# Optimization experiments

Measured on AMD Instinct MI355X. Metric: run time of the kernel, lower is better.

## Reference

```python
import jax, jax.numpy as jnp
import numpy as np

N, K = 262144, 8
IN_F, H_F, OUT_F = 16, 128, 16
NEG_SLOPE = 0.01  # torch LeakyReLU default


def setup_inputs() -> dict:
    key = jax.random.key(0)
    ks = jax.random.split(key, 10)
    h = jax.random.normal(ks[0], (N, IN_F), dtype=jnp.float32)
    pos = jax.random.uniform(ks[1], (N, 3), dtype=jnp.float32)
    nbr_idx = jax.random.randint(ks[2], (N, K), 0, N)

    def xavier(k, shape):
        fan_in, fan_out = shape[0], shape[1]
        a = jnp.sqrt(6.0 / (fan_in + fan_out))
        return jax.random.uniform(k, shape, jnp.float32, -a, a)

    W0 = xavier(ks[3], (K * IN_F, H_F))
    b0 = xavier(ks[4], (1, H_F))
    W1 = xavier(ks[5], (K * H_F, H_F))
    b1 = xavier(ks[6], (1, H_F))
    W2 = xavier(ks[7], (K * H_F, OUT_F))
    b2 = xavier(ks[8], (1, OUT_F))
    return {"h": h, "pos": pos, "nbr_idx": nbr_idx,
            "W0": W0, "b0": b0, "W1": W1, "b1": b1, "W2": W2, "b2": b2}


def _layer(h, pos, nbr_idx, W, b, activation):
    # gather neighbor messages and positions: [N, K, F], [N, K, 3]
    msgs = h[nbr_idx]
    src_pos = pos[nbr_idx]
    diff = pos[:, None, :] - src_pos                       # [N, K, 3]
    dist = jnp.sqrt(jnp.sum(diff * diff, axis=2, keepdims=True))  # [N, K, 1]
    dist = jnp.where(dist == 0, jnp.float32(0.5), dist)
    wow = (msgs / dist).reshape(h.shape[0], -1)            # [N, K*F]
    out = wow @ W + b
    if activation:
        out = jnp.where(out >= 0, out, NEG_SLOPE * out)
    return out


def reference(h, pos, nbr_idx, W0, b0, W1, b1, W2, b2):
    h1 = _layer(h, pos, nbr_idx, W0, b0, False)   # input layer
    h2 = _layer(h1, pos, nbr_idx, W1, b1, True)   # hidden layer (LeakyReLU)
    h3 = _layer(h2, pos, nbr_idx, W2, b2, False)  # output layer
    return h3
```

## Files before the change

kernel.cpp:

```cpp
#include <hip/hip_runtime.h>
#include <hip/hip_fp16.h>


typedef _Float16 f16x8 __attribute__((ext_vector_type(8)));
typedef float f32x4 __attribute__((ext_vector_type(4)));

#define NNODES 262144

__global__ __launch_bounds__(256) void prep_all_kernel(
    const float* __restrict__ h, __half* __restrict__ h16,
    const float* __restrict__ pos, const int* __restrict__ nbr,
    __half* __restrict__ invd,
    const float* __restrict__ W0, __half* __restrict__ W0f,
    const float* __restrict__ W1, __half* __restrict__ W1f,
    const float* __restrict__ W2, __half* __restrict__ W2f) {
    const int b = blockIdx.x;
    const int t = threadIdx.x;
    if (b < 16384) {
        int i = b * 256 + t;
        h16[i] = __float2half(h[i]);
    } else if (b < 24576) {
        int e = (b - 16384) * 256 + t;
        int i = e >> 3;
        int n = nbr[e];
        float dx = pos[i * 3 + 0] - pos[n * 3 + 0];
        float dy = pos[i * 3 + 1] - pos[n * 3 + 1];
        float dz = pos[i * 3 + 2] - pos[n * 3 + 2];
        float d = sqrtf(dx * dx + dy * dy + dz * dz);
        if (d == 0.0f) d = 0.5f;
        invd[e] = __float2half((1.0f / d) * 0.00390625f);
    } else if (b < 24640) {
        int e = (b - 24576) * 256 + t;
        int j = e & 7;
        int lane = (e >> 3) & 63;
        int rest = e >> 9;
        int tt = rest % 8;
        int s = rest / 8;
        int k = s * 32 + (lane >> 4) * 8 + j;
        int n = tt * 16 + (lane & 15);
        W0f[e] = __float2half(W0[k * 128 + n]);
    } else if (b < 25152) {
        int e = (b - 24640) * 256 + t;
        int j = e & 7;
        int lane = (e >> 3) & 63;
        int rest = e >> 9;
        int tt = rest % 8;
        int s = rest / 8;
        int k = s * 32 + (lane >> 4) * 8 + j;
        int n = tt * 16 + (lane & 15);
        W1f[e] = __float2half(W1[k * 128 + n]);
    } else {
        int e = (b - 25152) * 256 + t;
        int j = e & 7;
        int lane = (e >> 3) & 63;
        int rest = e >> 9;
        int tt = rest % 8;
        int s = rest / 8;
        int k = s * 32 + (lane >> 4) * 8 + j;
        W2f[e] = __float2half(W2[(size_t)(tt * 128 + k) * 16 + (lane & 15)]);
    }
}

__global__ __launch_bounds__(256) void layer0_kernel(
    const __half* __restrict__ hprev, const __half* __restrict__ invd,
    const int* __restrict__ nbr, const __half* __restrict__ Wf,
    const float* __restrict__ bias, __half* __restrict__ outp) {
    __shared__ __align__(16) __half Bs[16384];

    const int tid = threadIdx.x;
    const int wave = tid >> 6;
    const int lane = tid & 63;
    const int quad = lane >> 4;
    const int lmod = lane & 15;
    const int mbase = blockIdx.x * 128 + wave * 16 + lmod;

    int idx[2][8];
    f16x8 invr[2];
#pragma unroll
    for (int mt = 0; mt < 2; ++mt) {
        const int m = mbase + mt * 64;
        const int4* nrow = (const int4*)(nbr + (size_t)m * 8);
        const int4 iA = nrow[0];
        const int4 iB = nrow[1];
        idx[mt][0] = iA.x; idx[mt][1] = iA.y; idx[mt][2] = iA.z; idx[mt][3] = iA.w;
        idx[mt][4] = iB.x; idx[mt][5] = iB.y; idx[mt][6] = iB.z; idx[mt][7] = iB.w;
        invr[mt] = *(const f16x8*)(invd + (size_t)m * 8);
    }

    f32x4 acc[2][8];
#pragma unroll
    for (int mt = 0; mt < 2; ++mt)
#pragma unroll
        for (int t = 0; t < 8; ++t) acc[mt][t] = f32x4{0.f, 0.f, 0.f, 0.f};

    {
        const uint4* src = (const uint4*)Wf;
        uint4* dst = (uint4*)Bs;
#pragma unroll
        for (int i = 0; i < 8; ++i) dst[i * 256 + tid] = src[i * 256 + tid];
    }
    __syncthreads();

#pragma unroll
    for (int s = 0; s < 4; ++s) {
        const int nb = 2 * s + (quad >> 1);
        f16x8 as[2];
#pragma unroll
        for (int mt = 0; mt < 2; ++mt) {
            f16x8 av = *(const f16x8*)(hprev + (size_t)idx[mt][nb] * 16 + (quad & 1) * 8);
            as[mt] = av * invr[mt][nb];
        }
#pragma unroll
        for (int t = 0; t < 8; ++t) {
            f16x8 b = *(const f16x8*)(Bs + ((size_t)(s * 8 + t) * 64 + lane) * 8);
#pragma unroll
            for (int mt = 0; mt < 2; ++mt)
                acc[mt][t] = __builtin_amdgcn_mfma_f32_16x16x32_f16(as[mt], b, acc[mt][t], 0, 0, 0);
        }
    }

    __syncthreads();
#pragma unroll
    for (int mt = 0; mt < 2; ++mt) {
#pragma unroll
        for (int t = 0; t < 8; ++t) {
            const int col = t * 16 + lmod;
            const float bv = bias[col];
#pragma unroll
            for (int rr = 0; rr < 4; ++rr) {
                const int lrow = mt * 64 + wave * 16 + quad * 4 + rr;
                float v = acc[mt][t][rr] * 256.0f + bv;
                Bs[lrow * 128 + col] = __float2half(v);
            }
        }
    }
    __syncthreads();
    {
        const int lrow = tid >> 1;
        const int cb = (tid & 1) * 64;
        __half* gdst = outp + (size_t)(blockIdx.x * 128 + lrow) * 128 + cb;
        const __half* lsrc = Bs + lrow * 128 + cb;
#pragma unroll
        for (int j = 0; j < 8; ++j)
            *(f16x8*)(gdst + j * 8) = *(const f16x8*)(lsrc + j * 8);
    }
}

__device__ __forceinline__ int off16(int seg, int row) {
    return seg * 64 + (row & ~15) + ((row ^ seg) & 15);
}

__global__ __launch_bounds__(256, 4) void layer1p_kernel(
    const __half* __restrict__ hprev, const __half* __restrict__ invd,
    const int* __restrict__ nbr, const __half* __restrict__ Wf,
    const __half* __restrict__ Wf2s, const float* __restrict__ bias,
    __half* __restrict__ Pout) {
    __shared__ __align__(16) __half As[2][8192];

    const int tid = threadIdx.x;
    const int wave = tid >> 6;
    const int lane = tid & 63;
    const int quad = lane >> 4;
    const int lmod = lane & 15;
    const int rowblk = blockIdx.x * 64;
    const int seg = lmod;

    const int rbase = rowblk + wave * 16 + quad;
    const int* nbp = nbr + (size_t)rbase * 8;
    const __half* ivp = invd + (size_t)rbase * 8;

    const int sbase = lmod * 64 + wave * 16;

    int roff4[4];
#pragma unroll
    for (int ks = 0; ks < 4; ++ks) {
        const int sg = ks * 4 + quad;
        roff4[ks] = (sg * 64 + ((lmod ^ sg) & 15)) * 8;
    }

    const __half* WfB = Wf + ((size_t)(wave * 2) * 64 + lane) * 8;

    f16x8 Bc[2][2], Bn[2][2];
#pragma unroll
    for (int ks2 = 0; ks2 < 2; ++ks2)
#pragma unroll
        for (int tl = 0; tl < 2; ++tl)
            Bc[ks2][tl] = *(const f16x8*)(WfB + (size_t)(ks2 * 8 + tl) * 512);

    f16x8 ga[2][4];
    {
        int id0[4], id1[4];
#pragma unroll
        for (int i = 0; i < 4; ++i) id0[i] = nbp[i * 32 + 0];
#pragma unroll
        for (int i = 0; i < 4; ++i)
            ga[0][i] = *(const f16x8*)(hprev + (size_t)id0[i] * 128 + seg * 8);
#pragma unroll
        for (int i = 0; i < 4; ++i) id1[i] = nbp[i * 32 + 1];
#pragma unroll
        for (int i = 0; i < 4; ++i)
            ga[1][i] = *(const f16x8*)(hprev + (size_t)id1[i] * 128 + seg * 8);
    }

#pragma unroll
    for (int i = 0; i < 4; ++i) {
        const _Float16 sc = *(const _Float16*)(ivp + i * 32 + 0);
        f16x8 v = ga[0][i] * sc;
        *(f16x8*)(&As[0][(sbase + (((i * 4 + quad) ^ lmod) & 15)) * 8]) = v;
    }
    __syncthreads();

    f32x4 acc[4][2];
#pragma unroll
    for (int m = 0; m < 4; ++m) { acc[m][0] = f32x4{0.f,0.f,0.f,0.f}; acc[m][1] = f32x4{0.f,0.f,0.f,0.f}; }

#pragma unroll
    for (int nb = 0; nb < 8; ++nb) {
        const int cur = nb & 1;
        if (nb < 6) {
            int idn[4];
#pragma unroll
            for (int i = 0; i < 4; ++i) idn[i] = nbp[i * 32 + nb + 2];
#pragma unroll
            for (int i = 0; i < 4; ++i)
                ga[cur][i] = *(const f16x8*)(hprev + (size_t)idn[i] * 128 + seg * 8);
        }
#pragma unroll
        for (int h = 0; h < 2; ++h) {
            const int p = nb * 2 + h;
            if (p < 15) {
#pragma unroll
                for (int ks2 = 0; ks2 < 2; ++ks2)
#pragma unroll
                    for (int tl = 0; tl < 2; ++tl)
                        Bn[ks2][tl] = *(const f16x8*)(WfB + (size_t)(((p + 1) * 2 + ks2) * 8 + tl) * 512);
            }
#pragma unroll
            for (int m = 0; m < 4; ++m) {
#pragma unroll
                for (int ks2 = 0; ks2 < 2; ++ks2) {
                    f16x8 a = *(const f16x8*)(&As[cur][roff4[h * 2 + ks2] + m * 128]);
                    acc[m][0] = __builtin_amdgcn_mfma_f32_16x16x32_f16(a, Bc[ks2][0], acc[m][0], 0, 0, 0);
                    acc[m][1] = __builtin_amdgcn_mfma_f32_16x16x32_f16(a, Bc[ks2][1], acc[m][1], 0, 0, 0);
                }
            }
#pragma unroll
            for (int ks2 = 0; ks2 < 2; ++ks2) {
                Bc[ks2][0] = Bn[ks2][0];
                Bc[ks2][1] = Bn[ks2][1];
            }
        }
        if (nb < 7) {
#pragma unroll
            for (int i = 0; i < 4; ++i) {
                const _Float16 sc = *(const _Float16*)(ivp + i * 32 + nb + 1);
                f16x8 v = ga[(nb + 1) & 1][i] * sc;
                *(f16x8*)(&As[cur ^ 1][(sbase + (((i * 4 + quad) ^ lmod) & 15)) * 8]) = v;
            }
            __syncthreads();
        }
    }

    __half* As0 = &As[0][0];
#pragma unroll
    for (int m = 0; m < 4; ++m) {
#pragma unroll
        for (int tl = 0; tl < 2; ++tl) {
            const int col = wave * 32 + tl * 16 + lmod;
            const float bv = bias[col];
            const int sg = col >> 3;
            const int jj = col & 7;
#pragma unroll
            for (int rr = 0; rr < 4; ++rr) {
                const int row = m * 16 + quad * 4 + rr;
                float v = acc[m][tl][rr] * 256.0f + bv;
                v = (v >= 0.f) ? v : 0.01f * v;
                As0[off16(sg, row) * 8 + jj] = __float2half(v);
            }
        }
    }
    __syncthreads();

    const __half* WfB2 = Wf2s + ((size_t)(wave * 2) * 64 + lane) * 8;
    f16x8 B2[4][2];
#pragma unroll
    for (int ks = 0; ks < 4; ++ks)
#pragma unroll
        for (int tl = 0; tl < 2; ++tl)
            B2[ks][tl] = *(const f16x8*)(WfB2 + (size_t)(ks * 8 + tl) * 512);

    f32x4 acc2[4][2];
#pragma unroll
    for (int m = 0; m < 4; ++m) { acc2[m][0] = f32x4{0.f,0.f,0.f,0.f}; acc2[m][1] = f32x4{0.f,0.f,0.f,0.f}; }
#pragma unroll
    for (int m = 0; m < 4; ++m) {
#pragma unroll
        for (int ks = 0; ks < 4; ++ks) {
            f16x8 a2 = *(const f16x8*)(&As0[roff4[ks] + m * 128]);
            acc2[m][0] = __builtin_amdgcn_mfma_f32_16x16x32_f16(a2, B2[ks][0], acc2[m][0], 0, 0, 0);
            acc2[m][1] = __builtin_amdgcn_mfma_f32_16x16x32_f16(a2, B2[ks][1], acc2[m][1], 0, 0, 0);
        }
    }

#pragma unroll
    for (int m = 0; m < 4; ++m) {
#pragma unroll
        for (int tl = 0; tl < 2; ++tl) {
            const int col = wave * 32 + tl * 16 + lmod;
#pragma unroll
            for (int rr = 0; rr < 4; ++rr) {
                const int grow = rowblk + m * 16 + quad * 4 + rr;
                Pout[(size_t)grow * 128 + col] = __float2half(acc2[m][tl][rr]);
            }
        }
    }
}

__global__ __launch_bounds__(256) void reduce_kernel(
    const __half* __restrict__ P, const __half* __restrict__ invd,
    const int* __restrict__ nbr, const float* __restrict__ b2,
    float* __restrict__ outp) {
    const int t = blockIdx.x * 256 + threadIdx.x;
    const int d = t >> 1;
    const int half = t & 1;

    const int4* nrow = (const int4*)(nbr + (size_t)d * 8);
    const int4 iA = nrow[0];
    const int4 iB = nrow[1];
    const int idx[8] = {iA.x, iA.y, iA.z, iA.w, iB.x, iB.y, iB.z, iB.w};
    const f16x8 iv = *(const f16x8*)(invd + (size_t)d * 8);

    f16x8 v[8];
#pragma unroll
    for (int k = 0; k < 8; ++k)
        v[k] = *(const f16x8*)(P + (size_t)idx[k] * 128 + k * 16 + half * 8);

    float acc[8];
#pragma unroll
    for (int c = 0; c < 8; ++c) acc[c] = 0.f;
#pragma unroll
    for (int k = 0; k < 8; ++k) {
        const float w = (float)iv[k];
#pragma unroll
        for (int c = 0; c < 8; ++c) acc[c] += w * (float)v[k][c];
    }

    const float* bp = b2 + half * 8;
    float4 o[2];
#pragma unroll
    for (int q = 0; q < 2; ++q) {
        o[q].x = acc[q * 4 + 0] * 256.0f + bp[q * 4 + 0];
        o[q].y = acc[q * 4 + 1] * 256.0f + bp[q * 4 + 1];
        o[q].z = acc[q * 4 + 2] * 256.0f + bp[q * 4 + 2];
        o[q].w = acc[q * 4 + 3] * 256.0f + bp[q * 4 + 3];
    }
    float4* dst = (float4*)(outp + (size_t)d * 16 + half * 8);
    dst[0] = o[0];
    dst[1] = o[1];
}

extern "C" void kernel_launch(void* const* d_in, const int* in_sizes, int n_in,
                              void* d_out, int out_size, void* d_ws, size_t ws_size,
                              hipStream_t stream) {
    const float* h   = (const float*)d_in[0];
    const float* pos = (const float*)d_in[1];
    const int*   nbr = (const int*)d_in[2];
    const float* W0  = (const float*)d_in[3];
    const float* b0  = (const float*)d_in[4];
    const float* W1  = (const float*)d_in[5];
    const float* b1  = (const float*)d_in[6];
    const float* W2  = (const float*)d_in[7];
    const float* b2  = (const float*)d_in[8];

    const int N = NNODES;

    char* w = (char*)d_ws;
    __half* h1 = (__half*)w;
    __half* P  = (__half*)(w + (size_t)67108864);
    __half* invd2 = (__half*)w;

    char* ob = (char*)d_out;
    __half* invd = (__half*)(ob + 0);
    __half* h16  = (__half*)(ob + 4194304);
    __half* W0f  = (__half*)(ob + 12582912);
    __half* W1f  = (__half*)(ob + 12615680);
    __half* Wf2s = (__half*)(ob + 12877824);

    prep_all_kernel<<<25216, 256, 0, stream>>>(h, h16, pos, nbr, invd,
                                               W0, W0f, W1, W1f, W2, Wf2s);

    layer0_kernel<<<N / 128, 256, 0, stream>>>(h16, invd, nbr, W0f, b0, h1);
    layer1p_kernel<<<N / 64, 256, 0, stream>>>(h1, invd, nbr, W1f, Wf2s, b1, P);

    (void)hipMemcpyAsync(invd2, invd, 4194304, hipMemcpyDeviceToDevice, stream);

    reduce_kernel<<<(N * 2) / 256, 256, 0, stream>>>(P, invd2, nbr, b2, (float*)d_out);
}
```

Measured before the change: 312.1 us.

## Split layer1p work across 8 waves with one 16-column tile each

Doubles the layer1p block to 512 threads (8 waves). Each wave now computes a single 16-column output tile instead of two, and gathers 2 neighbor rows per step instead of 4. This lowers per-thread register use and spreads the gather loads and MFMA work over more waves to improve latency hiding. In exchange there are more waves per block contending at each barrier, and the B-fragment loads per block are duplicated across more waves.

```diff
diff --git a/kernel.cpp b/kernel.cpp
--- a/kernel.cpp
+++ b/kernel.cpp
@@ -150,7 +150,7 @@
     return seg * 64 + (row & ~15) + ((row ^ seg) & 15);
 }
 
-__global__ __launch_bounds__(256, 4) void layer1p_kernel(
+__global__ __launch_bounds__(512, 4) void layer1p_kernel(
     const __half* __restrict__ hprev, const __half* __restrict__ invd,
     const int* __restrict__ nbr, const __half* __restrict__ Wf,
     const __half* __restrict__ Wf2s, const float* __restrict__ bias,
@@ -165,11 +165,12 @@
     const int rowblk = blockIdx.x * 64;
     const int seg = lmod;
 
-    const int rbase = rowblk + wave * 16 + quad;
-    const int* nbp = nbr + (size_t)rbase * 8;
-    const __half* ivp = invd + (size_t)rbase * 8;
-
-    const int sbase = lmod * 64 + wave * 16;
+    const int r0 = wave * 4 + quad;
+    const int* nbp = nbr + (size_t)(rowblk + r0) * 8;
+    const __half* ivp = invd + (size_t)(rowblk + r0) * 8;
+
+    const int soff0 = off16(seg, r0) * 8;
+    const int soff1 = off16(seg, r0 + 32) * 8;
 
     int roff4[4];
 #pragma unroll
@@ -178,52 +179,45 @@
         roff4[ks] = (sg * 64 + ((lmod ^ sg) & 15)) * 8;
     }
 
-    const __half* WfB = Wf + ((size_t)(wave * 2) * 64 + lane) * 8;
-
-    f16x8 Bc[2][2], Bn[2][2];
+    const __half* WfB = Wf + ((size_t)wave * 64 + lane) * 8;
+
+    f16x8 Bc[2], Bn[2];
 #pragma unroll
     for (int ks2 = 0; ks2 < 2; ++ks2)
-#pragma unroll
-        for (int tl = 0; tl < 2; ++tl)
-            Bc[ks2][tl] = *(const f16x8*)(WfB + (size_t)(ks2 * 8 + tl) * 512);
-
-    f16x8 ga[2][4];
-    {
-        int id0[4], id1[4];
-#pragma unroll
-        for (int i = 0; i < 4; ++i) id0[i] = nbp[i * 32 + 0];
-#pragma unroll
-        for (int i = 0; i < 4; ++i)
-            ga[0][i] = *(const f16x8*)(hprev + (size_t)id0[i] * 128 + seg * 8);
-#pragma unroll
-        for (int i = 0; i < 4; ++i) id1[i] = nbp[i * 32 + 1];
-#pragma unroll
-        for (int i = 0; i < 4; ++i)
-            ga[1][i] = *(const f16x8*)(hprev + (size_t)id1[i] * 128 + seg * 8);
-    }
-
-#pragma unroll
-    for (int i = 0; i < 4; ++i) {
-        const _Float16 sc = *(const _Float16*)(ivp + i * 32 + 0);
-        f16x8 v = ga[0][i] * sc;
-        *(f16x8*)(&As[0][(sbase + (((i * 4 + quad) ^ lmod) & 15)) * 8]) = v;
-    }
-    __syncthreads();
-
-    f32x4 acc[4][2];
-#pragma unroll
-    for (int m = 0; m < 4; ++m) { acc[m][0] = f32x4{0.f,0.f,0.f,0.f}; acc[m][1] = f32x4{0.f,0.f,0.f,0.f}; }
+        Bc[ks2] = *(const f16x8*)(WfB + (size_t)ks2 * 4096);
+
+    f16x8 ga[2][2];
+    {
+        int id0[2], id1[2];
+        id0[0] = nbp[0];   id0[1] = nbp[256];
+        ga[0][0] = *(const f16x8*)(hprev + (size_t)id0[0] * 128 + seg * 8);
+        ga[0][1] = *(const f16x8*)(hprev + (size_t)id0[1] * 128 + seg * 8);
+        id1[0] = nbp[1];   id1[1] = nbp[257];
+        ga[1][0] = *(const f16x8*)(hprev + (size_t)id1[0] * 128 + seg * 8);
+        ga[1][1] = *(const f16x8*)(hprev + (size_t)id1[1] * 128 + seg * 8);
+    }
+
+    {
+        const _Float16 s0 = *(const _Float16*)(ivp + 0);
+        const _Float16 s1 = *(const _Float16*)(ivp + 256);
+        *(f16x8*)(&As[0][soff0]) = ga[0][0] * s0;
+        *(f16x8*)(&As[0][soff1]) = ga[0][1] * s1;
+    }
+    __syncthreads();
+
+    f32x4 acc[4];
+#pragma unroll
+    for (int m = 0; m < 4; ++m) acc[m] = f32x4{0.f, 0.f, 0.f, 0.f};
 
 #pragma unroll
     for (int nb = 0; nb < 8; ++nb) {
         const int cur = nb & 1;
         if (nb < 6) {
-            int idn[4];
-#pragma unroll
-            for (int i = 0; i < 4; ++i) idn[i] = nbp[i * 32 + nb + 2];
-#pragma unroll
-            for (int i = 0; i < 4; ++i)
-                ga[cur][i] = *(const f16x8*)(hprev + (size_t)idn[i] * 128 + seg * 8);
+            int idn[2];
+            idn[0] = nbp[nb + 2];
+            idn[1] = nbp[nb + 258];
+            ga[cur][0] = *(const f16x8*)(hprev + (size_t)idn[0] * 128 + seg * 8);
+            ga[cur][1] = *(const f16x8*)(hprev + (size_t)idn[1] * 128 + seg * 8);
         }
 #pragma unroll
         for (int h = 0; h < 2; ++h) {
@@ -231,49 +225,40 @@
             if (p < 15) {
 #pragma unroll
                 for (int ks2 = 0; ks2 < 2; ++ks2)
-#pragma unroll
-                    for (int tl = 0; tl < 2; ++tl)
-                        Bn[ks2][tl] = *(const f16x8*)(WfB + (size_t)(((p + 1) * 2 + ks2) * 8 + tl) * 512);
+                    Bn[ks2] = *(const f16x8*)(WfB + (size_t)((p + 1) * 2 + ks2) * 4096);
             }
 #pragma unroll
             for (int m = 0; m < 4; ++m) {
 #pragma unroll
                 for (int ks2 = 0; ks2 < 2; ++ks2) {
                     f16x8 a = *(const f16x8*)(&As[cur][roff4[h * 2 + ks2] + m * 128]);
-                    acc[m][0] = __builtin_amdgcn_mfma_f32_16x16x32_f16(a, Bc[ks2][0], acc[m][0], 0, 0, 0);
-                    acc[m][1] = __builtin_amdgcn_mfma_f32_16x16x32_f16(a, Bc[ks2][1], acc[m][1], 0, 0, 0);
+                    acc[m] = __builtin_amdgcn_mfma_f32_16x16x32_f16(a, Bc[ks2], acc[m], 0, 0, 0);
                 }
             }
-#pragma unroll
-            for (int ks2 = 0; ks2 < 2; ++ks2) {
-                Bc[ks2][0] = Bn[ks2][0];
-                Bc[ks2][1] = Bn[ks2][1];
-            }
+            Bc[0] = Bn[0];
+            Bc[1] = Bn[1];
         }
         if (nb < 7) {
-#pragma unroll
-            for (int i = 0; i < 4; ++i) {
-                const _Float16 sc = *(const _Float16*)(ivp + i * 32 + nb + 1);
-                f16x8 v = ga[(nb + 1) & 1][i] * sc;
-                *(f16x8*)(&As[cur ^ 1][(sbase + (((i * 4 + quad) ^ lmod) & 15)) * 8]) = v;
-            }
+            const _Float16 s0 = *(const _Float16*)(ivp + nb + 1);
+            const _Float16 s1 = *(const _Float16*)(ivp + nb + 257);
+            *(f16x8*)(&As[cur ^ 1][soff0]) = ga[(nb + 1) & 1][0] * s0;
+            *(f16x8*)(&As[cur ^ 1][soff1]) = ga[(nb + 1) & 1][1] * s1;
             __syncthreads();
         }
     }
 
     __half* As0 = &As[0][0];
-#pragma unroll
-    for (int m = 0; m < 4; ++m) {
-#pragma unroll
-        for (int tl = 0; tl < 2; ++tl) {
-            const int col = wave * 32 + tl * 16 + lmod;
-            const float bv = bias[col];
-            const int sg = col >> 3;
-            const int jj = col & 7;
+    {
+        const int col = wave * 16 + lmod;
+        const float bv = bias[col];
+        const int sg = col >> 3;
+        const int jj = col & 7;
+#pragma unroll
+        for (int m = 0; m < 4; ++m) {
 #pragma unroll
             for (int rr = 0; rr < 4; ++rr) {
                 const int row = m * 16 + quad * 4 + rr;
-                float v = acc[m][tl][rr] * 256.0f + bv;
+                float v = acc[m][rr] * 256.0f + bv;
                 v = (v >= 0.f) ? v : 0.01f * v;
                 As0[off16(sg, row) * 8 + jj] = __float2half(v);
             }
@@ -281,36 +266,32 @@
     }
     __syncthreads();
 
-    const __half* WfB2 = Wf2s + ((size_t)(wave * 2) * 64 + lane) * 8;
-    f16x8 B2[4][2];
+    const __half* WfB2 = Wf2s + ((size_t)wave * 64 + lane) * 8;
+    f16x8 B2[4];
 #pragma unroll
     for (int ks = 0; ks < 4; ++ks)
-#pragma unroll
-        for (int tl = 0; tl < 2; ++tl)
-            B2[ks][tl] = *(const f16x8*)(WfB2 + (size_t)(ks * 8 + tl) * 512);
-
-    f32x4 acc2[4][2];
-#pragma unroll
-    for (int m = 0; m < 4; ++m) { acc2[m][0] = f32x4{0.f,0.f,0.f,0.f}; acc2[m][1] = f32x4{0.f,0.f,0.f,0.f}; }
+        B2[ks] = *(const f16x8*)(WfB2 + (size_t)ks * 4096);
+
+    f32x4 acc2[4];
+#pragma unroll
+    for (int m = 0; m < 4; ++m) acc2[m] = f32x4{0.f, 0.f, 0.f, 0.f};
 #pragma unroll
     for (int m = 0; m < 4; ++m) {
 #pragma unroll
         for (int ks = 0; ks < 4; ++ks) {
             f16x8 a2 = *(const f16x8*)(&As0[roff4[ks] + m * 128]);
-            acc2[m][0] = __builtin_amdgcn_mfma_f32_16x16x32_f16(a2, B2[ks][0], acc2[m][0], 0, 0, 0);
-            acc2[m][1] = __builtin_amdgcn_mfma_f32_16x16x32_f16(a2, B2[ks][1], acc2[m][1], 0, 0, 0);
-        }
-    }
-
-#pragma unroll
-    for (int m = 0; m < 4; ++m) {
-#pragma unroll
-        for (int tl = 0; tl < 2; ++tl) {
-            const int col = wave * 32 + tl * 16 + lmod;
+            acc2[m] = __builtin_amdgcn_mfma_f32_16x16x32_f16(a2, B2[ks], acc2[m], 0, 0, 0);
+        }
+    }
+
+    {
+        const int col = wave * 16 + lmod;
+#pragma unroll
+        for (int m = 0; m < 4; ++m) {
 #pragma unroll
             for (int rr = 0; rr < 4; ++rr) {
                 const int grow = rowblk + m * 16 + quad * 4 + rr;
-                Pout[(size_t)grow * 128 + col] = __float2half(acc2[m][tl][rr]);
+                Pout[(size_t)grow * 128 + col] = __float2half(acc2[m][rr]);
             }
         }
     }
@@ -390,7 +371,7 @@
                                                W0, W0f, W1, W1f, W2, Wf2s);
 
     layer0_kernel<<<N / 128, 256, 0, stream>>>(h16, invd, nbr, W0f, b0, h1);
-    layer1p_kernel<<<N / 64, 256, 0, stream>>>(h1, invd, nbr, W1f, Wf2s, b1, P);
+    layer1p_kernel<<<N / 64, 512, 0, stream>>>(h1, invd, nbr, W1f, Wf2s, b1, P);
 
     (void)hipMemcpyAsync(invd2, invd, 4194304, hipMemcpyDeviceToDevice, stream);
 
```

Measured after the change: 313.7 us. Within noise of the previous version (+0.5%).
